# Kernel tuning notes

Measured on AMD Instinct MI355X. Metric: run time of the kernel, lower is better.

## Reference

```python
import jax, jax.numpy as jnp
import numpy as np

NEG = jnp.float32(-1e30)  # max-plus identity (finite to keep grads clean)


def setup_inputs() -> dict:
    key = jax.random.key(0)
    k1, k2 = jax.random.split(key)
    B, Cin, H, W = 8, 64, 64, 64
    Cout, kH, kW = 64, 3, 3
    x = jax.random.normal(k1, (B, Cin, H, W), dtype=jnp.float32)
    weight = jax.random.normal(k2, (Cout, Cin, kH, kW), dtype=jnp.float32)
    return {"x": x, "weight": weight, "kernel_size": 3, "padding": 1}


def reference(x, weight, kernel_size, padding):
    # Max-plus correlation (tropical conv), stride 1:
    #   out[b,co,y,x] = max_{ci,i,j} ( x_pad[b,ci,y+i,x+j] + weight[co,ci,i,j] )
    kH = kW = int(kernel_size)
    padH = padW = int(padding)
    B, Cin, H, W = x.shape
    Cout = weight.shape[0]
    xp = jnp.pad(x, ((0, 0), (0, 0), (padH, padH), (padW, padW)),
                 constant_values=NEG)  # -inf-like padding: identity of max
    Ho = H + 2 * padH - kH + 1
    Wo = W + 2 * padW - kW + 1
    out = jnp.full((B, Cout, Ho, Wo), NEG, dtype=x.dtype)
    for i in range(kH):          # small fixed kernel loop (kH*kW taps)
        for j in range(kW):
            win = xp[:, :, i:i + Ho, j:j + Wo]            # [B,Ci,Ho,Wo]
            cand = win[:, None] + weight[None, :, :, i, j, None, None]
            out = jnp.maximum(out, cand.max(axis=2))      # reduce over Ci
    return out
```

## Files before the change

kernel.cpp:

```cpp
#include <hip/hip_runtime.h>

#define NEGV -1e30f

constexpr int Bn = 8, Ci = 64, Hn = 64, Wn = 64, Co = 64;
constexpr int WT_ELEMS = Ci * 9 * Co;
constexpr int HW = Hn * Wn;

__global__ __launch_bounds__(256)
void wtrans_kernel(const float* __restrict__ wt, float* __restrict__ wT) {
    int idx = blockIdx.x * 256 + threadIdx.x;
    if (idx < WT_ELEMS) {
        int co = idx & 63;
        int k  = (idx >> 6) % 9;
        int ci = idx / 576;
        wT[idx] = wt[((size_t)co * Ci + ci) * 9 + k];
    }
}

__device__ __forceinline__ float vmax3(float a, float b, float c) {
    float d;
    asm("v_max3_f32 %0, %1, %2, %3" : "=v"(d) : "v"(a), "v"(b), "v"(c));
    return d;
}

__device__ __forceinline__ void read10(float* o, const float* __restrict__ p) {
    float4 a = *reinterpret_cast<const float4*>(p);
    float4 b = *reinterpret_cast<const float4*>(p + 4);
    float2 c = *reinterpret_cast<const float2*>(p + 8);
    o[0] = a.x; o[1] = a.y; o[2] = a.z; o[3] = a.w;
    o[4] = b.x; o[5] = b.y; o[6] = b.z; o[7] = b.w;
    o[8] = c.x; o[9] = c.y;
}

__device__ __forceinline__ void compute8(float* acc, const float* xu,
                                         const float* xc, const float* xd,
                                         const float* wv) {
#pragma unroll
    for (int j = 0; j < 8; j++) {
        float t0 = xu[j] + wv[0], t1 = xu[j + 1] + wv[1], t2 = xu[j + 2] + wv[2];
        float t3 = xc[j] + wv[3], t4 = xc[j + 1] + wv[4], t5 = xc[j + 2] + wv[5];
        float t6 = xd[j] + wv[6], t7 = xd[j + 1] + wv[7], t8 = xd[j + 2] + wv[8];
        float m0 = vmax3(t0, t1, t2);
        float m1 = vmax3(t3, t4, t5);
        float m2 = vmax3(t6, t7, t8);
        acc[j] = vmax3(acc[j], m0, m1);
        acc[j] = fmaxf(acc[j], m2);
    }
}

__global__ __launch_bounds__(512, 8)
void maxconv_main(const float* __restrict__ x, const float* __restrict__ wT,
                  float* __restrict__ out) {
    __shared__ __align__(16) float xs[Ci * 120];

    const int tid  = threadIdx.x;
    const int lane = tid & 63;
    const int wid  = tid >> 6;

    const int lg   = ((blockIdx.x & 7) << 7) | (blockIdx.x >> 3);
    const int b    = lg >> 7;
    const int rem  = lg & 127;
    const int h    = rem >> 1;
    const int half = rem & 1;
    const int w0h  = half << 5;

    {
        const int q      = tid >> 7;
        const int st     = tid & 127;
        const int cibase = q * 16;
        if (st < 102) {
            const int r    = st / 34;
            const int s    = st - r * 34;
            const int grow = h - 1 + r;
            const int gcol = w0h - 1 + s;
            const bool valid = (grow >= 0) && (grow < Hn) && (gcol >= 0) && (gcol < Wn);
            const int cg   = valid ? grow : 0;
            const int cc   = valid ? gcol : 0;
            const float* gp = x + (((size_t)b * Ci + cibase) * Hn + cg) * Wn + cc;
            const int dst  = r * 40 + s;
#pragma unroll 1
            for (int c8 = 0; c8 < 16; c8 += 8) {
                float v[8];
#pragma unroll
                for (int i = 0; i < 8; i++)
                    v[i] = valid ? gp[(size_t)(c8 + i) * HW] : NEGV;
#pragma unroll
                for (int i = 0; i < 8; i++)
                    xs[(cibase + c8 + i) * 120 + dst] = v[i];
            }
        }
    }
    __syncthreads();

    const int quad   = wid >> 1;
    const int cihalf = wid & 1;
    const int woff   = quad * 8;

    const float* wq = wT + (size_t)cihalf * 32 * 576 + lane;
    const float* xq = xs + cihalf * 32 * 120 + woff;

    float acc[8];
#pragma unroll
    for (int j = 0; j < 8; j++) acc[j] = NEGV;

#pragma unroll 1
    for (int ci = 0; ci < 32; ci += 2) {
        float wv[9];
#pragma unroll
        for (int k = 0; k < 9; k++) wv[k] = wq[k * 64];
        float xu[10], xc[10], xd[10];
        read10(xu, xq); read10(xc, xq + 40); read10(xd, xq + 80);
        compute8(acc, xu, xc, xd, wv);
        wq += 576; xq += 120;

        float wv2[9];
#pragma unroll
        for (int k = 0; k < 9; k++) wv2[k] = wq[k * 64];
        float yu[10], yc[10], yd[10];
        read10(yu, xq); read10(yc, xq + 40); read10(yd, xq + 80);
        compute8(acc, yu, yc, yd, wv2);
        wq += 576; xq += 120;
    }

    __syncthreads();
    if (cihalf) {
        float* ps = xs + quad * 512 + lane * 8;
        *reinterpret_cast<float4*>(ps)     = make_float4(acc[0], acc[1], acc[2], acc[3]);
        *reinterpret_cast<float4*>(ps + 4) = make_float4(acc[4], acc[5], acc[6], acc[7]);
    }
    __syncthreads();
    if (!cihalf) {
        const float* ps = xs + quad * 512 + lane * 8;
        float4 o0 = *reinterpret_cast<const float4*>(ps);
        float4 o1 = *reinterpret_cast<const float4*>(ps + 4);
        acc[0] = fmaxf(acc[0], o0.x); acc[1] = fmaxf(acc[1], o0.y);
        acc[2] = fmaxf(acc[2], o0.z); acc[3] = fmaxf(acc[3], o0.w);
        acc[4] = fmaxf(acc[4], o1.x); acc[5] = fmaxf(acc[5], o1.y);
        acc[6] = fmaxf(acc[6], o1.z); acc[7] = fmaxf(acc[7], o1.w);

        float* po = out + (((size_t)b * Co + lane) * Hn + h) * Wn + w0h + woff;
        *reinterpret_cast<float4*>(po)     = make_float4(acc[0], acc[1], acc[2], acc[3]);
        *reinterpret_cast<float4*>(po + 4) = make_float4(acc[4], acc[5], acc[6], acc[7]);
    }
}

extern "C" void kernel_launch(void* const* d_in, const int* in_sizes, int n_in,
                              void* d_out, int out_size, void* d_ws, size_t ws_size,
                              hipStream_t stream) {
    const float* x  = (const float*)d_in[0];
    const float* wt = (const float*)d_in[1];
    float* out = (float*)d_out;
    float* wT  = (float*)d_ws;

    wtrans_kernel<<<(WT_ELEMS + 255) / 256, 256, 0, stream>>>(wt, wT);

    maxconv_main<<<1024, 512, 0, stream>>>(x, wT, out);
}
```

Baseline: 113.2 us.

## Compute two output rows per block to reuse weights and shared input rows

Each block now produces two adjacent output rows instead of one. It loads a 4-row halo tile per channel and reuses each weight load and the middle input rows across both rows' accumulators. This halves the grid to 512 blocks and cuts per-output weight loads and LDS reads. In exchange it raises register use and LDS per block (occupancy hint lowered to 4), and leaves fewer blocks to spread across the CUs.

```diff
diff --git a/kernel.cpp b/kernel.cpp
--- a/kernel.cpp
+++ b/kernel.cpp
@@ -48,46 +48,45 @@
     }
 }
 
-__global__ __launch_bounds__(512, 8)
+__global__ __launch_bounds__(512, 4)
 void maxconv_main(const float* __restrict__ x, const float* __restrict__ wT,
                   float* __restrict__ out) {
-    __shared__ __align__(16) float xs[Ci * 120];
+    __shared__ __align__(16) float xs[Ci * 160];
 
     const int tid  = threadIdx.x;
     const int lane = tid & 63;
     const int wid  = tid >> 6;
 
-    const int lg   = ((blockIdx.x & 7) << 7) | (blockIdx.x >> 3);
-    const int b    = lg >> 7;
-    const int rem  = lg & 127;
-    const int h    = rem >> 1;
+    const int lg   = ((blockIdx.x & 7) << 6) | (blockIdx.x >> 3);
+    const int b    = lg >> 6;
+    const int rem  = lg & 63;
+    const int pair = rem >> 1;
     const int half = rem & 1;
+    const int h0   = pair * 2;
     const int w0h  = half << 5;
 
-    {
-        const int q      = tid >> 7;
-        const int st     = tid & 127;
-        const int cibase = q * 16;
-        if (st < 102) {
-            const int r    = st / 34;
-            const int s    = st - r * 34;
-            const int grow = h - 1 + r;
-            const int gcol = w0h - 1 + s;
-            const bool valid = (grow >= 0) && (grow < Hn) && (gcol >= 0) && (gcol < Wn);
-            const int cg   = valid ? grow : 0;
-            const int cc   = valid ? gcol : 0;
-            const float* gp = x + (((size_t)b * Ci + cibase) * Hn + cg) * Wn + cc;
-            const int dst  = r * 40 + s;
+    for (int u = tid; u < 544; u += 512) {
+        const int ciq  = u / 136;
+        const int r2   = u - ciq * 136;
+        const int r    = r2 / 34;
+        const int s    = r2 - r * 34;
+        const int cibase = ciq * 16;
+        const int grow = h0 - 1 + r;
+        const int gcol = w0h - 1 + s;
+        const bool valid = (grow >= 0) && (grow < Hn) && (gcol >= 0) && (gcol < Wn);
+        const int cg   = valid ? grow : 0;
+        const int cc   = valid ? gcol : 0;
+        const float* gp = x + (((size_t)b * Ci + cibase) * Hn + cg) * Wn + cc;
+        const int dst  = r * 40 + s;
 #pragma unroll 1
-            for (int c8 = 0; c8 < 16; c8 += 8) {
-                float v[8];
+        for (int c8 = 0; c8 < 16; c8 += 8) {
+            float v[8];
 #pragma unroll
-                for (int i = 0; i < 8; i++)
-                    v[i] = valid ? gp[(size_t)(c8 + i) * HW] : NEGV;
+            for (int i = 0; i < 8; i++)
+                v[i] = valid ? gp[(size_t)(c8 + i) * HW] : NEGV;
 #pragma unroll
-                for (int i = 0; i < 8; i++)
-                    xs[(cibase + c8 + i) * 120 + dst] = v[i];
-            }
+            for (int i = 0; i < 8; i++)
+                xs[(cibase + c8 + i) * 160 + dst] = v[i];
         }
     }
     __syncthreads();
@@ -97,50 +96,54 @@
     const int woff   = quad * 8;
 
     const float* wq = wT + (size_t)cihalf * 32 * 576 + lane;
-    const float* xq = xs + cihalf * 32 * 120 + woff;
+    const float* xq = xs + cihalf * 32 * 160 + woff;
 
-    float acc[8];
+    float acc0[8], acc1[8];
 #pragma unroll
-    for (int j = 0; j < 8; j++) acc[j] = NEGV;
+    for (int j = 0; j < 8; j++) { acc0[j] = NEGV; acc1[j] = NEGV; }
 
 #pragma unroll 1
-    for (int ci = 0; ci < 32; ci += 2) {
+    for (int ci = 0; ci < 32; ci++) {
         float wv[9];
 #pragma unroll
         for (int k = 0; k < 9; k++) wv[k] = wq[k * 64];
-        float xu[10], xc[10], xd[10];
-        read10(xu, xq); read10(xc, xq + 40); read10(xd, xq + 80);
-        compute8(acc, xu, xc, xd, wv);
-        wq += 576; xq += 120;
-
-        float wv2[9];
-#pragma unroll
-        for (int k = 0; k < 9; k++) wv2[k] = wq[k * 64];
-        float yu[10], yc[10], yd[10];
-        read10(yu, xq); read10(yc, xq + 40); read10(yd, xq + 80);
-        compute8(acc, yu, yc, yd, wv2);
-        wq += 576; xq += 120;
+        float r0[10], r1[10], r2[10], r3[10];
+        read10(r0, xq);       read10(r1, xq + 40);
+        read10(r2, xq + 80);  read10(r3, xq + 120);
+        compute8(acc0, r0, r1, r2, wv);
+        compute8(acc1, r1, r2, r3, wv);
+        wq += 576; xq += 160;
     }
 
     __syncthreads();
     if (cihalf) {
-        float* ps = xs + quad * 512 + lane * 8;
-        *reinterpret_cast<float4*>(ps)     = make_float4(acc[0], acc[1], acc[2], acc[3]);
-        *reinterpret_cast<float4*>(ps + 4) = make_float4(acc[4], acc[5], acc[6], acc[7]);
+        float* ps = xs + quad * 1024 + lane * 16;
+        *reinterpret_cast<float4*>(ps)      = make_float4(acc0[0], acc0[1], acc0[2], acc0[3]);
+        *reinterpret_cast<float4*>(ps + 4)  = make_float4(acc0[4], acc0[5], acc0[6], acc0[7]);
+        *reinterpret_cast<float4*>(ps + 8)  = make_float4(acc1[0], acc1[1], acc1[2], acc1[3]);
+        *reinterpret_cast<float4*>(ps + 12) = make_float4(acc1[4], acc1[5], acc1[6], acc1[7]);
     }
     __syncthreads();
     if (!cihalf) {
-        const float* ps = xs + quad * 512 + lane * 8;
+        const float* ps = xs + quad * 1024 + lane * 16;
         float4 o0 = *reinterpret_cast<const float4*>(ps);
         float4 o1 = *reinterpret_cast<const float4*>(ps + 4);
-        acc[0] = fmaxf(acc[0], o0.x); acc[1] = fmaxf(acc[1], o0.y);
-        acc[2] = fmaxf(acc[2], o0.z); acc[3] = fmaxf(acc[3], o0.w);
-        acc[4] = fmaxf(acc[4], o1.x); acc[5] = fmaxf(acc[5], o1.y);
-        acc[6] = fmaxf(acc[6], o1.z); acc[7] = fmaxf(acc[7], o1.w);
+        float4 o2 = *reinterpret_cast<const float4*>(ps + 8);
+        float4 o3 = *reinterpret_cast<const float4*>(ps + 12);
+        acc0[0] = fmaxf(acc0[0], o0.x); acc0[1] = fmaxf(acc0[1], o0.y);
+        acc0[2] = fmaxf(acc0[2], o0.z); acc0[3] = fmaxf(acc0[3], o0.w);
+        acc0[4] = fmaxf(acc0[4], o1.x); acc0[5] = fmaxf(acc0[5], o1.y);
+        acc0[6] = fmaxf(acc0[6], o1.z); acc0[7] = fmaxf(acc0[7], o1.w);
+        acc1[0] = fmaxf(acc1[0], o2.x); acc1[1] = fmaxf(acc1[1], o2.y);
+        acc1[2] = fmaxf(acc1[2], o2.z); acc1[3] = fmaxf(acc1[3], o2.w);
+        acc1[4] = fmaxf(acc1[4], o3.x); acc1[5] = fmaxf(acc1[5], o3.y);
+        acc1[6] = fmaxf(acc1[6], o3.z); acc1[7] = fmaxf(acc1[7], o3.w);
 
-        float* po = out + (((size_t)b * Co + lane) * Hn + h) * Wn + w0h + woff;
-        *reinterpret_cast<float4*>(po)     = make_float4(acc[0], acc[1], acc[2], acc[3]);
-        *reinterpret_cast<float4*>(po + 4) = make_float4(acc[4], acc[5], acc[6], acc[7]);
+        float* po = out + (((size_t)b * Co + lane) * Hn + h0) * Wn + w0h + woff;
+        *reinterpret_cast<float4*>(po)          = make_float4(acc0[0], acc0[1], acc0[2], acc0[3]);
+        *reinterpret_cast<float4*>(po + 4)      = make_float4(acc0[4], acc0[5], acc0[6], acc0[7]);
+        *reinterpret_cast<float4*>(po + Wn)     = make_float4(acc1[0], acc1[1], acc1[2], acc1[3]);
+        *reinterpret_cast<float4*>(po + Wn + 4) = make_float4(acc1[4], acc1[5], acc1[6], acc1[7]);
     }
 }
 
@@ -154,5 +157,5 @@
 
     wtrans_kernel<<<(WT_ELEMS + 255) / 256, 256, 0, stream>>>(wt, wT);
 
-    maxconv_main<<<1024, 512, 0, stream>>>(x, wT, out);
+    maxconv_main<<<512, 512, 0, stream>>>(x, wT, out);
 }
```

Result: no change. 112.3 us, median of 2 (-0.8%).
